# Kernel tuning notes

Hardware: AMD Instinct MI355X
Metric: run time of the kernel (lower is better)

The kernel has to match this reference:

```python
import jax, jax.numpy as jnp
import numpy as np

D_MODEL, HEADS, D_FF = 768, 12, 3072
D_K = D_MODEL // HEADS
EPS = 1e-6


def _norm(x, alpha, bias):
    # NormalizationLayer: scalar alpha/bias, torch.std is unbiased (ddof=1)
    mean = jnp.mean(x, axis=-1, keepdims=True)
    std = jnp.std(x, axis=-1, ddof=1, keepdims=True)
    return alpha * (x - mean) / (std + EPS) + bias


def setup_inputs() -> dict:
    key = jax.random.key(0)
    ks = jax.random.split(key, 16)
    B, S = 2, 4096
    x = jax.random.normal(ks[0], (B, S, D_MODEL), dtype=jnp.float32)
    mask = jax.random.randint(ks[1], (B, 1, 1, S), 0, 2, dtype=jnp.int32)
    w = lambda k, o, i: (jax.random.normal(k, (o, i), dtype=jnp.float32) * 0.02)
    return {
        "x": x, "mask": mask,
        "wq": w(ks[2], D_MODEL, D_MODEL), "bq": jnp.zeros((D_MODEL,), jnp.float32),
        "wk": w(ks[3], D_MODEL, D_MODEL), "bk": jnp.zeros((D_MODEL,), jnp.float32),
        "wv": w(ks[4], D_MODEL, D_MODEL), "bv": jnp.zeros((D_MODEL,), jnp.float32),
        "wo": w(ks[5], D_MODEL, D_MODEL), "bo": jnp.zeros((D_MODEL,), jnp.float32),
        "w1": w(ks[6], D_FF, D_MODEL), "b1": jnp.zeros((D_FF,), jnp.float32),
        "w2": w(ks[7], D_MODEL, D_FF), "b2": jnp.zeros((D_MODEL,), jnp.float32),
        "alpha1": jnp.ones((1,), jnp.float32), "beta1": jnp.ones((1,), jnp.float32),
        "alpha2": jnp.ones((1,), jnp.float32), "beta2": jnp.ones((1,), jnp.float32),
    }


def reference(x, mask, wq, bq, wk, bk, wv, bv, wo, bo, w1, b1, w2, b2,
              alpha1, beta1, alpha2, beta2):
    B, S, _ = x.shape

    # --- residual connection 0: pre-norm + self-attention ---
    h = _norm(x, alpha1, beta1)
    q = (h @ wq.T + bq).reshape(B, S, HEADS, D_K).transpose(0, 2, 1, 3)  # [B,H,S,dk]
    k = (h @ wk.T + bk).reshape(B, S, HEADS, D_K).transpose(0, 2, 1, 3)
    v = (h @ wv.T + bv).reshape(B, S, HEADS, D_K).transpose(0, 2, 1, 3)
    scores = jnp.einsum('bhqd,bhkd->bhqk', q, k) / jnp.sqrt(jnp.float32(D_K))
    scores = jnp.where(mask == 0, jnp.float32(-1e9), scores)
    attn = jax.nn.softmax(scores, axis=-1)
    ctx = jnp.einsum('bhqk,bhkd->bhqd', attn, v)
    ctx = ctx.transpose(0, 2, 1, 3).reshape(B, S, D_MODEL)
    x = x + (ctx @ wo.T + bo)

    # --- residual connection 1: pre-norm + FFN ---
    h = _norm(x, alpha2, beta2)
    ff = jax.nn.relu(h @ w1.T + b1) @ w2.T + b2
    return x + ff
```

## Files before the change

### kernel.cpp

```cpp
#include <hip/hip_runtime.h>
#include <hip/hip_bf16.h>
#include <math.h>


typedef __hip_bfloat16 bf16;
typedef short short8 __attribute__((ext_vector_type(8)));
typedef short short4v __attribute__((ext_vector_type(4)));
typedef float f32x4 __attribute__((ext_vector_type(4)));

#define MFMA(A, B, C) __builtin_amdgcn_mfma_f32_16x16x32_bf16(A, B, C, 0, 0, 0)

#if __has_builtin(__builtin_amdgcn_exp2f)
#define EXP2(x) __builtin_amdgcn_exp2f(x)
#else
#define EXP2(x) exp2f(x)
#endif

__device__ __forceinline__ void gl_lds16(const void* g, void* l) {
  __builtin_amdgcn_global_load_lds(
      (__attribute__((address_space(1))) void*)g,
      (__attribute__((address_space(3))) void*)l, 16, 0, 0);
}

__device__ __forceinline__ short f2b(float f) {
  bf16 h = __float2bfloat16(f);
  return *reinterpret_cast<short*>(&h);
}

__global__ __launch_bounds__(256)
void prep_all(const float* __restrict__ wq, const float* __restrict__ wk,
              const float* __restrict__ wv, const float* __restrict__ wo,
              const float* __restrict__ w1, const float* __restrict__ w2,
              const float* __restrict__ bq, const float* __restrict__ bk,
              const float* __restrict__ bv, const int* __restrict__ mask,
              bf16* __restrict__ wqkvb, bf16* __restrict__ wob,
              bf16* __restrict__ w1b, bf16* __restrict__ w2b,
              float* __restrict__ bqkv,
              int* __restrict__ pos_g, int* __restrict__ nch_g,
              float* __restrict__ biasc,
              bf16* __restrict__ kc, bf16* __restrict__ vtc)
{
  const int t = threadIdx.x;
  if (blockIdx.x < 2) {
    const int b = blockIdx.x;
    const int* mb = mask + b * 4096;
    __shared__ int lsum[256];
    int loc = 0;
    int mv[16];
#pragma unroll
    for (int j = 0; j < 16; j++) { mv[j] = mb[t * 16 + j] ? 1 : 0; loc += mv[j]; }
    lsum[t] = loc;
    __syncthreads();
    for (int off = 1; off < 256; off <<= 1) {
      int v = (t >= off) ? lsum[t - off] : 0;
      __syncthreads();
      lsum[t] += v;
      __syncthreads();
    }
    const int nvalid = lsum[255];
    int base = lsum[t] - loc;
#pragma unroll
    for (int j = 0; j < 16; j++) {
      pos_g[b * 4096 + t * 16 + j] = mv[j] ? base : -1;
      if (mv[j]) base++;
    }
    const int npad = (nvalid + 63) & ~63;
    if (t == 0) nch_g[b] = npad >> 6;
    for (int i = t; i < 4096; i += 256)
      biasc[b * 4096 + i] = (i < nvalid) ? 0.f : -1e9f;
    const int npv = npad - nvalid;
    if (npv > 0) {
      const int krows = 12 * npv;
      const short8 z = {};
      for (int task = t; task < krows * 8; task += 256) {
        const int rr = task >> 3, cc = task & 7;
        const int hh = rr / npv, r = nvalid + rr % npv;
        *(short8*)&kc[(((long)(b * 12 + hh) * 4096) + r) * 64 + cc * 8] = z;
      }
      const int vrows = 12 * 64;
      for (int task = t; task < vrows * npv; task += 256) {
        const int row = task / npv, j = nvalid + task % npv;
        const int hh = row >> 6, d = row & 63;
        vtc[((long)((b * 12 + hh) * 64 + d)) * 4096 + j] = __float2bfloat16(0.f);
      }
    }
    return;
  }
  const int i = (blockIdx.x - 2) * 256 + t;
  const int W = 147456;
  const int F = 589824;
  const float* src; bf16* dst; int off;
  if (i < W)          { src = wq; dst = wqkvb;           off = i; }
  else if (i < 2*W)   { src = wk; dst = wqkvb + 589824;  off = i - W; }
  else if (i < 3*W)   { src = wv; dst = wqkvb + 1179648; off = i - 2*W; }
  else if (i < 4*W)   { src = wo; dst = wob;             off = i - 3*W; }
  else if (i < 4*W+F) { src = w1; dst = w1b;             off = i - 4*W; }
  else                { src = w2; dst = w2b;             off = i - 4*W - F; }
  float4 v = ((const float4*)src)[off];
  short4v o;
  o.x = f2b(v.x); o.y = f2b(v.y); o.z = f2b(v.z); o.w = f2b(v.w);
  ((short4v*)dst)[off] = o;
  if (i < 2304)
    bqkv[i] = (i < 768) ? bq[i] : (i < 1536 ? bk[i - 768] : bv[i - 1536]);
}

template<typename INT>
__global__ __launch_bounds__(256)
void ln_kernel(const INT* __restrict__ x, bf16* __restrict__ out,
               const float* __restrict__ alpha, const float* __restrict__ beta)
{
  const int row = blockIdx.x;
  const long base = (long)row * 768;
  const int t = threadIdx.x;
  float v[3]; float s = 0.f, ss = 0.f;
#pragma unroll
  for (int i = 0; i < 3; i++) {
    v[i] = (float)x[base + t + i * 256];
    s += v[i]; ss += v[i] * v[i];
  }
#pragma unroll
  for (int off = 32; off > 0; off >>= 1) {
    s  += __shfl_down(s, off);
    ss += __shfl_down(ss, off);
  }
  __shared__ float red[8];
  __shared__ float stats[2];
  const int w = t >> 6;
  if ((t & 63) == 0) { red[w] = s; red[4 + w] = ss; }
  __syncthreads();
  if (t == 0) {
    float S  = red[0] + red[1] + red[2] + red[3];
    float SS = red[4] + red[5] + red[6] + red[7];
    float mean = S * (1.f / 768.f);
    float var = fmaxf((SS - 768.f * mean * mean) * (1.f / 767.f), 0.f);
    stats[0] = mean;
    stats[1] = 1.f / (sqrtf(var) + 1e-6f);
  }
  __syncthreads();
  const float mean = stats[0], rinv = stats[1];
  const float a = alpha[0], b = beta[0];
#pragma unroll
  for (int i = 0; i < 3; i++)
    out[base + t + i * 256] = __float2bfloat16(a * (v[i] - mean) * rinv + b);
}

template<int MODE, int TM, typename RT, typename OUTT>
__global__ __launch_bounds__(256)
void gemm_bt(const bf16* __restrict__ A, const bf16* __restrict__ W,
             const float* __restrict__ bias, const RT* __restrict__ R,
             OUTT* __restrict__ Cout, int M, int N, int K)
{
  constexpr int MI = TM / 32;
  __shared__ __align__(16) bf16 sA[TM * 32];
  __shared__ __align__(16) bf16 sB[128 * 32];
  const int t = threadIdx.x;
  const int w = t >> 6, lane = t & 63;
  const int lr = lane & 15, quad = lane >> 4;
  const int tm = blockIdx.x * TM, tn = blockIdx.y * 128;
  const int wm = (w >> 1) * (MI * 16), wn = (w & 1) * 64;

  const int srow = w * 16 + (lane >> 2);
  const int scol = (lane & 3) * 8;
  const bf16* Ap = A + (long)(tm + srow) * K + scol;
  const bf16* Wp = W + (long)(tn + srow) * K + scol;
  bf16* sAp = &sA[srow * 32 + scol];
  bf16* sBp = &sB[srow * 32 + scol];
  const long half = (long)64 * K;

  f32x4 acc[MI][4] = {};

  for (int kb = 0; kb < K; kb += 32) {
    gl_lds16(Ap + kb, sAp);
    if (TM == 128) gl_lds16(Ap + kb + half, sAp + 64 * 32);
    gl_lds16(Wp + kb, sBp);
    gl_lds16(Wp + kb + half, sBp + 64 * 32);
    __syncthreads();
    short8 af[MI], bfr[4];
#pragma unroll
    for (int i = 0; i < MI; i++)
      af[i] = *(const short8*)&sA[(wm + i * 16 + lr) * 32 + quad * 8];
#pragma unroll
    for (int j = 0; j < 4; j++)
      bfr[j] = *(const short8*)&sB[(wn + j * 16 + lr) * 32 + quad * 8];
#pragma unroll
    for (int i = 0; i < MI; i++)
#pragma unroll
      for (int j = 0; j < 4; j++)
        acc[i][j] = MFMA(af[i], bfr[j], acc[i][j]);
    __syncthreads();
  }

#pragma unroll
  for (int i = 0; i < MI; i++) {
#pragma unroll
    for (int j = 0; j < 4; j++) {
      const int col = tn + wn + j * 16 + lr;
      const float bv = bias[col];
#pragma unroll
      for (int r = 0; r < 4; r++) {
        const int m = tm + wm + i * 16 + quad * 4 + r;
        float vv = acc[i][j][r] + bv;
        if (MODE == 1) vv = fmaxf(vv, 0.f);
        if (MODE == 4) vv += (float)R[(long)m * N + col];
        Cout[(long)m * N + col] = (OUTT)vv;
      }
    }
  }
}

__global__ __launch_bounds__(256)
void gemm_qkv(const bf16* __restrict__ A, const bf16* __restrict__ W,
              const float* __restrict__ bias, const int* __restrict__ pos_g,
              bf16* __restrict__ Qo, bf16* __restrict__ Kc, bf16* __restrict__ Vtc)
{
  const int K = 768;
  __shared__ __align__(16) bf16 sA[128 * 32];
  __shared__ __align__(16) bf16 sB[128 * 32];
  const int t = threadIdx.x;
  const int w = t >> 6, lane = t & 63;
  const int lr = lane & 15, quad = lane >> 4;
  const int tm = blockIdx.x * 128, tn = blockIdx.y * 128;
  const int wm = (w >> 1) * 64, wn = (w & 1) * 64;

  const int srow = w * 16 + (lane >> 2);
  const int scol = (lane & 3) * 8;
  const bf16* Ap = A + (long)(tm + srow) * K + scol;
  const bf16* Wp = W + (long)(tn + srow) * K + scol;
  bf16* sAp = &sA[srow * 32 + scol];
  bf16* sBp = &sB[srow * 32 + scol];
  const long half = (long)64 * K;

  f32x4 acc[4][4] = {};

  for (int kb = 0; kb < K; kb += 32) {
    gl_lds16(Ap + kb, sAp);
    gl_lds16(Ap + kb + half, sAp + 64 * 32);
    gl_lds16(Wp + kb, sBp);
    gl_lds16(Wp + kb + half, sBp + 64 * 32);
    __syncthreads();
    short8 af[4], bfr[4];
#pragma unroll
    for (int i = 0; i < 4; i++)
      af[i] = *(const short8*)&sA[(wm + i * 16 + lr) * 32 + quad * 8];
#pragma unroll
    for (int j = 0; j < 4; j++)
      bfr[j] = *(const short8*)&sB[(wn + j * 16 + lr) * 32 + quad * 8];
#pragma unroll
    for (int i = 0; i < 4; i++)
#pragma unroll
      for (int j = 0; j < 4; j++)
        acc[i][j] = MFMA(af[i], bfr[j], acc[i][j]);
    __syncthreads();
  }

  const int region = (tn >= 1536) ? 2 : (tn >= 768 ? 1 : 0);
#pragma unroll
  for (int i = 0; i < 4; i++) {
#pragma unroll
    for (int j = 0; j < 4; j++) {
      const int col = tn + wn + j * 16 + lr;
      const int c768 = col - region * 768;
      const int hh = c768 >> 6, d = c768 & 63;
      const float bv = bias[col];
#pragma unroll
      for (int r = 0; r < 4; r++) {
        const int m = tm + wm + i * 16 + quad * 4 + r;
        const int bb = m >> 12, sdx = m & 4095;
        float vv = acc[i][j][r] + bv;
        if (region == 0) {
          vv *= 0.18033688011112042f;
          Qo[((long)(bb * 12 + hh) * 4096 + sdx) * 64 + d] = __float2bfloat16(vv);
        } else {
          const int p_ = pos_g[bb * 4096 + sdx];
          if (p_ >= 0) {
            if (region == 1)
              Kc[((long)(bb * 12 + hh) * 4096 + p_) * 64 + d] = __float2bfloat16(vv);
            else
              Vtc[((long)(bb * 12 + hh) * 64 + d) * 4096 + p_] = __float2bfloat16(vv);
          }
        }
      }
    }
  }
}

__global__ __launch_bounds__(256)
void attn_kernel(const bf16* __restrict__ Q, const bf16* __restrict__ Kg,
                 const bf16* __restrict__ Vt, const float* __restrict__ biasc,
                 const int* __restrict__ nch_g, bf16* __restrict__ ctx)
{
  __shared__ __align__(16) bf16 sK[2][64 * 64];
  __shared__ __align__(16) bf16 sV[2][64 * 64];
  __shared__ __align__(16) bf16 sP[4][32 * 64];

  const int t = threadIdx.x, w = t >> 6, lane = t & 63;
  const int lr = lane & 15, quad = lane >> 4;
  const int bh = blockIdx.y, b = bh / 12, hh = bh % 12;
  const int qb = blockIdx.x * 128 + w * 32;
  const long bh_s = (long)bh * 4096;
  const float* bg = biasc + b * 4096;
  const int nch = nch_g[b];
  bf16* sPw = sP[w];

  short8 qf[2][2];
#pragma unroll
  for (int qt = 0; qt < 2; qt++) {
    const bf16* qp = Q + (bh_s + qb + qt * 16 + lr) * 64 + quad * 8;
    qf[qt][0] = *(const short8*)qp;
    qf[qt][1] = *(const short8*)(qp + 32);
  }

  const int rA = w * 16 + (lane >> 3), rB = rA + 8;
  const int c8 = lane & 7;
  const int sigA = ((rA & 15) << 2) + (rA >> 4);
  const int sigB = ((rB & 15) << 2) + (rB >> 4);
  const bf16* kA = Kg + (bh_s + sigA) * 64 + ((c8 ^ (rA & 7)) << 3);
  const bf16* kB = Kg + (bh_s + sigB) * 64 + ((c8 ^ (rB & 7)) << 3);
  const bf16* vA = Vt + ((long)bh * 64 + rA) * 4096 + ((c8 ^ (rA & 7)) << 3);
  const bf16* vB = Vt + ((long)bh * 64 + rB) * 4096 + ((c8 ^ (rB & 7)) << 3);
  const int ldsA = (w * 16) * 64 + lane * 8;
  const int ldsB = ldsA + 8 * 64;

  const int cA = (quad * 8) ^ ((lr & 7) << 3);

  float l_part[2][4] = {};
  f32x4 O[2][4] = {};

  auto stage = [&](int kc, int buf) {
    gl_lds16(kA + (long)kc * 64, &sK[buf][ldsA]);
    gl_lds16(kB + (long)kc * 64, &sK[buf][ldsB]);
    gl_lds16(vA + kc, &sV[buf][ldsA]);
    gl_lds16(vB + kc, &sV[buf][ldsB]);
  };

  auto compute = [&](int kc, int buf, bool dobias) {
    const bf16* Kb = sK[buf];
    const bf16* Vb = sV[buf];
    f32x4 s[2][4] = {};
#pragma unroll
    for (int kt = 0; kt < 4; kt++) {
      const int rowb = (kt * 16 + lr) * 64;
      short8 kfa = *(const short8*)&Kb[rowb + cA];
      short8 kfb = *(const short8*)&Kb[rowb + (cA ^ 32)];
      s[0][kt] = MFMA(qf[0][0], kfa, s[0][kt]);
      s[0][kt] = MFMA(qf[0][1], kfb, s[0][kt]);
      s[1][kt] = MFMA(qf[1][0], kfa, s[1][kt]);
      s[1][kt] = MFMA(qf[1][1], kfb, s[1][kt]);
    }
    float bb0 = 0.f, bb1 = 0.f, bb2 = 0.f, bb3 = 0.f;
    if (dobias) {
      const float4 b4 = *(const float4*)&bg[kc + lr * 4];
      bb0 = b4.x; bb1 = b4.y; bb2 = b4.z; bb3 = b4.w;
    }
#pragma unroll
    for (int qt = 0; qt < 2; qt++) {
#pragma unroll
      for (int r = 0; r < 4; r++) {
        float p0, p1, p2, p3;
        if (dobias) {
          p0 = EXP2(s[qt][0][r] + bb0); p1 = EXP2(s[qt][1][r] + bb1);
          p2 = EXP2(s[qt][2][r] + bb2); p3 = EXP2(s[qt][3][r] + bb3);
        } else {
          p0 = EXP2(s[qt][0][r]); p1 = EXP2(s[qt][1][r]);
          p2 = EXP2(s[qt][2][r]); p3 = EXP2(s[qt][3][r]);
        }
        l_part[qt][r] += (p0 + p1) + (p2 + p3);
        const int q = qt * 16 + quad * 4 + r;
        short4v pw;
        pw.x = f2b(p0); pw.y = f2b(p1); pw.z = f2b(p2); pw.w = f2b(p3);
        *(short4v*)&sPw[q * 64 + ((lr * 4) ^ ((q & 7) << 3))] = pw;
      }
    }
    short8 pf[2][2];
#pragma unroll
    for (int qt = 0; qt < 2; qt++) {
      const int rowb = (qt * 16 + lr) * 64;
      pf[qt][0] = *(const short8*)&sPw[rowb + cA];
      pf[qt][1] = *(const short8*)&sPw[rowb + (cA ^ 32)];
    }
#pragma unroll
    for (int j = 0; j < 4; j++) {
      const int rowb = (j * 16 + lr) * 64;
      short8 vfa = *(const short8*)&Vb[rowb + cA];
      short8 vfb = *(const short8*)&Vb[rowb + (cA ^ 32)];
      O[0][j] = MFMA(pf[0][0], vfa, O[0][j]);
      O[0][j] = MFMA(pf[0][1], vfb, O[0][j]);
      O[1][j] = MFMA(pf[1][0], vfa, O[1][j]);
      O[1][j] = MFMA(pf[1][1], vfb, O[1][j]);
    }
  };

  stage(0, 0);
  for (int ci = 0; ci < nch - 1; ci++) {
    __syncthreads();
    stage((ci + 1) * 64, (ci + 1) & 1);
    compute(ci * 64, ci & 1, false);
  }
  __syncthreads();
  if (nch > 0) compute((nch - 1) * 64, (nch - 1) & 1, true);

#pragma unroll
  for (int qt = 0; qt < 2; qt++) {
#pragma unroll
    for (int r = 0; r < 4; r++) {
      float l = l_part[qt][r];
#pragma unroll
      for (int off = 1; off < 16; off <<= 1) l += __shfl_xor(l, off, 16);
      const float il = (l > 0.f) ? 1.f / l : 0.f;
      const int q = qb + qt * 16 + quad * 4 + r;
      bf16* cp = ctx + ((long)(b * 4096 + q)) * 768 + hh * 64 + lr;
#pragma unroll
      for (int j = 0; j < 4; j++)
        cp[j * 16] = __float2bfloat16(O[qt][j][r] * il);
    }
  }
}

extern "C" void kernel_launch(void* const* d_in, const int* in_sizes, int n_in,
                              void* d_out, int out_size, void* d_ws, size_t ws_size,
                              hipStream_t stream)
{
  (void)in_sizes; (void)n_in; (void)out_size; (void)ws_size;
  const float* x    = (const float*)d_in[0];
  const int*   mask = (const int*)  d_in[1];
  const float* wq = (const float*)d_in[2];  const float* bq = (const float*)d_in[3];
  const float* wk = (const float*)d_in[4];  const float* bk = (const float*)d_in[5];
  const float* wv = (const float*)d_in[6];  const float* bv = (const float*)d_in[7];
  const float* wo = (const float*)d_in[8];  const float* bo = (const float*)d_in[9];
  const float* w1 = (const float*)d_in[10]; const float* b1 = (const float*)d_in[11];
  const float* w2 = (const float*)d_in[12]; const float* b2 = (const float*)d_in[13];
  const float* alpha1 = (const float*)d_in[14]; const float* beta1 = (const float*)d_in[15];
  const float* alpha2 = (const float*)d_in[16]; const float* beta2 = (const float*)d_in[17];
  float* out = (float*)d_out;

  const long WSZ = (long)768 * 768 * 2;
  const long W1SZ = (long)3072 * 768 * 2;
  const long SZB = (long)8192 * 768 * 2;
  char* ws = (char*)d_ws;
  bf16* wqkvb = (bf16*)(ws);
  bf16* wob = (bf16*)(ws + 3 * WSZ);
  bf16* w1b = (bf16*)(ws + 4 * WSZ);
  bf16* w2b = (bf16*)(ws + 4 * WSZ + W1SZ);
  char* aux = ws + 4 * WSZ + 2 * W1SZ;
  float* bqkv   = (float*)(aux);
  int*   pos_g  = (int*)(aux + 16384);
  float* biasc  = (float*)(aux + 49152);
  int*   nch_g  = (int*)(aux + 81920);
  const long BASE = 16l << 20;
  bf16* h   = (bf16*)(ws + BASE);
  bf16* qws = (bf16*)(ws + BASE + 1 * SZB);
  bf16* kcw = (bf16*)(ws + BASE + 2 * SZB);
  bf16* vtc = (bf16*)(ws + BASE + 3 * SZB);
  bf16* ctx = (bf16*)(ws + BASE + 4 * SZB);
  bf16* x1  = (bf16*)(ws + BASE + 5 * SZB);
  bf16* ff  = qws;

  dim3 blk(256);

  hipLaunchKernelGGL(prep_all, dim3(6914), blk, 0, stream,
                     wq, wk, wv, wo, w1, w2, bq, bk, bv, mask,
                     wqkvb, wob, w1b, w2b, bqkv, pos_g, nch_g, biasc, kcw, vtc);

  hipLaunchKernelGGL((ln_kernel<float>), dim3(8192), blk, 0, stream, x, h, alpha1, beta1);
  hipLaunchKernelGGL(gemm_qkv, dim3(64, 18), blk, 0, stream, h, wqkvb, bqkv, pos_g, qws, kcw, vtc);
  hipLaunchKernelGGL(attn_kernel, dim3(32, 24), blk, 0, stream, qws, kcw, vtc, biasc, nch_g, ctx);
  hipLaunchKernelGGL((gemm_bt<4, 64, float, bf16>), dim3(128, 6), blk, 0, stream, ctx, wob, bo, x, x1, 8192, 768, 768);
  hipLaunchKernelGGL((ln_kernel<bf16>), dim3(8192), blk, 0, stream, x1, h, alpha2, beta2);
  hipLaunchKernelGGL((gemm_bt<1, 128, float, bf16>), dim3(64, 24), blk, 0, stream, h, w1b, b1, (const float*)nullptr, ff, 8192, 3072, 768);
  hipLaunchKernelGGL((gemm_bt<4, 64, bf16, float>), dim3(128, 6), blk, 0, stream, ff, w2b, b2, x1, out, 8192, 768, 3072);
}
```

Baseline: 407.3 us.

## Keep attention probabilities in registers via transposed MFMA and permlane swaps

The attention kernel now computes S^T and O^T by swapping the MFMA operands, then repacks the bf16 probabilities with v_cvt_pk and v_permlane16/32 swaps. This lets them feed the PV MFMA straight from registers instead of taking a round trip through per-wave LDS. The padding bias on the last chunk is replaced by zero-padded K rows, whose exp2(0)=1 contributions are subtracted from the row sum using a stored padding count. s_setprio hints are added around the MFMA sections. The risks are reliance on gfx950-specific permlane instructions and on an exact correction for the padded keys.

```diff
diff --git a/kernel.cpp b/kernel.cpp
--- a/kernel.cpp
+++ b/kernel.cpp
@@ -15,6 +15,15 @@
 #else
 #define EXP2(x) exp2f(x)
 #endif
+
+#define PSWAP32(a, b) asm("v_permlane32_swap_b32 %0, %1" : "+v"(a), "+v"(b))
+#define PSWAP16(a, b) asm("v_permlane16_swap_b32 %0, %1" : "+v"(a), "+v"(b))
+
+__device__ __forceinline__ unsigned cvt_pk(float lo, float hi) {
+  unsigned r;
+  asm("v_cvt_pk_bf16_f32 %0, %1, %2" : "=v"(r) : "v"(lo), "v"(hi));
+  return r;
+}
 
 __device__ __forceinline__ void gl_lds16(const void* g, void* l) {
   __builtin_amdgcn_global_load_lds(
@@ -37,7 +46,6 @@
               bf16* __restrict__ w1b, bf16* __restrict__ w2b,
               float* __restrict__ bqkv,
               int* __restrict__ pos_g, int* __restrict__ nch_g,
-              float* __restrict__ biasc,
               bf16* __restrict__ kc, bf16* __restrict__ vtc)
 {
   const int t = threadIdx.x;
@@ -65,9 +73,7 @@
       if (mv[j]) base++;
     }
     const int npad = (nvalid + 63) & ~63;
-    if (t == 0) nch_g[b] = npad >> 6;
-    for (int i = t; i < 4096; i += 256)
-      biasc[b * 4096 + i] = (i < nvalid) ? 0.f : -1e9f;
+    if (t == 0) { nch_g[b * 2] = npad >> 6; nch_g[b * 2 + 1] = npad - nvalid; }
     const int npv = npad - nvalid;
     if (npv > 0) {
       const int krows = 12 * npv;
@@ -286,21 +292,19 @@
 
 __global__ __launch_bounds__(256)
 void attn_kernel(const bf16* __restrict__ Q, const bf16* __restrict__ Kg,
-                 const bf16* __restrict__ Vt, const float* __restrict__ biasc,
+                 const bf16* __restrict__ Vt,
                  const int* __restrict__ nch_g, bf16* __restrict__ ctx)
 {
   __shared__ __align__(16) bf16 sK[2][64 * 64];
   __shared__ __align__(16) bf16 sV[2][64 * 64];
-  __shared__ __align__(16) bf16 sP[4][32 * 64];
 
   const int t = threadIdx.x, w = t >> 6, lane = t & 63;
   const int lr = lane & 15, quad = lane >> 4;
   const int bh = blockIdx.y, b = bh / 12, hh = bh % 12;
   const int qb = blockIdx.x * 128 + w * 32;
   const long bh_s = (long)bh * 4096;
-  const float* bg = biasc + b * 4096;
-  const int nch = nch_g[b];
-  bf16* sPw = sP[w];
+  const int nch = nch_g[b * 2];
+  const int npv = nch_g[b * 2 + 1];
 
   short8 qf[2][2];
 #pragma unroll
@@ -312,10 +316,8 @@
 
   const int rA = w * 16 + (lane >> 3), rB = rA + 8;
   const int c8 = lane & 7;
-  const int sigA = ((rA & 15) << 2) + (rA >> 4);
-  const int sigB = ((rB & 15) << 2) + (rB >> 4);
-  const bf16* kA = Kg + (bh_s + sigA) * 64 + ((c8 ^ (rA & 7)) << 3);
-  const bf16* kB = Kg + (bh_s + sigB) * 64 + ((c8 ^ (rB & 7)) << 3);
+  const bf16* kA = Kg + (bh_s + rA) * 64 + ((c8 ^ (rA & 7)) << 3);
+  const bf16* kB = Kg + (bh_s + rB) * 64 + ((c8 ^ (rB & 7)) << 3);
   const bf16* vA = Vt + ((long)bh * 64 + rA) * 4096 + ((c8 ^ (rA & 7)) << 3);
   const bf16* vB = Vt + ((long)bh * 64 + rB) * 4096 + ((c8 ^ (rB & 7)) << 3);
   const int ldsA = (w * 16) * 64 + lane * 8;
@@ -323,8 +325,8 @@
 
   const int cA = (quad * 8) ^ ((lr & 7) << 3);
 
-  float l_part[2][4] = {};
-  f32x4 O[2][4] = {};
+  float l_part[2] = {};
+  f32x4 Ot[4][2] = {};
 
   auto stage = [&](int kc, int buf) {
     gl_lds16(kA + (long)kc * 64, &sK[buf][ldsA]);
@@ -333,85 +335,90 @@
     gl_lds16(vB + kc, &sV[buf][ldsB]);
   };
 
-  auto compute = [&](int kc, int buf, bool dobias) {
+  auto compute = [&](int buf) {
     const bf16* Kb = sK[buf];
     const bf16* Vb = sV[buf];
-    f32x4 s[2][4] = {};
+    f32x4 st[4][2] = {};
+    __builtin_amdgcn_s_setprio(1);
 #pragma unroll
     for (int kt = 0; kt < 4; kt++) {
       const int rowb = (kt * 16 + lr) * 64;
       short8 kfa = *(const short8*)&Kb[rowb + cA];
       short8 kfb = *(const short8*)&Kb[rowb + (cA ^ 32)];
-      s[0][kt] = MFMA(qf[0][0], kfa, s[0][kt]);
-      s[0][kt] = MFMA(qf[0][1], kfb, s[0][kt]);
-      s[1][kt] = MFMA(qf[1][0], kfa, s[1][kt]);
-      s[1][kt] = MFMA(qf[1][1], kfb, s[1][kt]);
-    }
-    float bb0 = 0.f, bb1 = 0.f, bb2 = 0.f, bb3 = 0.f;
-    if (dobias) {
-      const float4 b4 = *(const float4*)&bg[kc + lr * 4];
-      bb0 = b4.x; bb1 = b4.y; bb2 = b4.z; bb3 = b4.w;
-    }
+      st[kt][0] = MFMA(kfa, qf[0][0], st[kt][0]);
+      st[kt][0] = MFMA(kfb, qf[0][1], st[kt][0]);
+      st[kt][1] = MFMA(kfa, qf[1][0], st[kt][1]);
+      st[kt][1] = MFMA(kfb, qf[1][1], st[kt][1]);
+    }
+    __builtin_amdgcn_s_setprio(0);
+
+    short8 pf[2][2];
 #pragma unroll
     for (int qt = 0; qt < 2; qt++) {
-#pragma unroll
-      for (int r = 0; r < 4; r++) {
-        float p0, p1, p2, p3;
-        if (dobias) {
-          p0 = EXP2(s[qt][0][r] + bb0); p1 = EXP2(s[qt][1][r] + bb1);
-          p2 = EXP2(s[qt][2][r] + bb2); p3 = EXP2(s[qt][3][r] + bb3);
-        } else {
-          p0 = EXP2(s[qt][0][r]); p1 = EXP2(s[qt][1][r]);
-          p2 = EXP2(s[qt][2][r]); p3 = EXP2(s[qt][3][r]);
+      float p[4][4];
+      float lp = 0.f;
+#pragma unroll
+      for (int kt = 0; kt < 4; kt++) {
+#pragma unroll
+        for (int r = 0; r < 4; r++) {
+          p[kt][r] = EXP2(st[kt][qt][r]);
+          lp += p[kt][r];
         }
-        l_part[qt][r] += (p0 + p1) + (p2 + p3);
-        const int q = qt * 16 + quad * 4 + r;
-        short4v pw;
-        pw.x = f2b(p0); pw.y = f2b(p1); pw.z = f2b(p2); pw.w = f2b(p3);
-        *(short4v*)&sPw[q * 64 + ((lr * 4) ^ ((q & 7) << 3))] = pw;
       }
-    }
-    short8 pf[2][2];
-#pragma unroll
-    for (int qt = 0; qt < 2; qt++) {
-      const int rowb = (qt * 16 + lr) * 64;
-      pf[qt][0] = *(const short8*)&sPw[rowb + cA];
-      pf[qt][1] = *(const short8*)&sPw[rowb + (cA ^ 32)];
-    }
-#pragma unroll
-    for (int j = 0; j < 4; j++) {
-      const int rowb = (j * 16 + lr) * 64;
+      l_part[qt] += lp;
+      unsigned u00 = cvt_pk(p[0][0], p[0][1]), u01 = cvt_pk(p[0][2], p[0][3]);
+      unsigned u10 = cvt_pk(p[1][0], p[1][1]), u11 = cvt_pk(p[1][2], p[1][3]);
+      unsigned u20 = cvt_pk(p[2][0], p[2][1]), u21 = cvt_pk(p[2][2], p[2][3]);
+      unsigned u30 = cvt_pk(p[3][0], p[3][1]), u31 = cvt_pk(p[3][2], p[3][3]);
+      PSWAP32(u00, u10); PSWAP32(u01, u11);
+      PSWAP32(u20, u30); PSWAP32(u21, u31);
+      PSWAP16(u00, u10); PSWAP16(u01, u11);
+      PSWAP16(u20, u30); PSWAP16(u21, u31);
+      union { unsigned u[4]; short8 s8; } fa, fb;
+      fa.u[0] = u00; fa.u[1] = u01; fa.u[2] = u10; fa.u[3] = u11;
+      fb.u[0] = u20; fb.u[1] = u21; fb.u[2] = u30; fb.u[3] = u31;
+      pf[qt][0] = fa.s8;
+      pf[qt][1] = fb.s8;
+    }
+
+    __builtin_amdgcn_s_setprio(1);
+#pragma unroll
+    for (int dt = 0; dt < 4; dt++) {
+      const int rowb = (dt * 16 + lr) * 64;
       short8 vfa = *(const short8*)&Vb[rowb + cA];
       short8 vfb = *(const short8*)&Vb[rowb + (cA ^ 32)];
-      O[0][j] = MFMA(pf[0][0], vfa, O[0][j]);
-      O[0][j] = MFMA(pf[0][1], vfb, O[0][j]);
-      O[1][j] = MFMA(pf[1][0], vfa, O[1][j]);
-      O[1][j] = MFMA(pf[1][1], vfb, O[1][j]);
-    }
+      Ot[dt][0] = MFMA(vfa, pf[0][0], Ot[dt][0]);
+      Ot[dt][0] = MFMA(vfb, pf[0][1], Ot[dt][0]);
+      Ot[dt][1] = MFMA(vfa, pf[1][0], Ot[dt][1]);
+      Ot[dt][1] = MFMA(vfb, pf[1][1], Ot[dt][1]);
+    }
+    __builtin_amdgcn_s_setprio(0);
   };
 
   stage(0, 0);
-  for (int ci = 0; ci < nch - 1; ci++) {
-    __syncthreads();
-    stage((ci + 1) * 64, (ci + 1) & 1);
-    compute(ci * 64, ci & 1, false);
-  }
-  __syncthreads();
-  if (nch > 0) compute((nch - 1) * 64, (nch - 1) & 1, true);
+  for (int ci = 0; ci < nch; ci++) {
+    __syncthreads();
+    if (ci + 1 < nch) stage((ci + 1) * 64, (ci + 1) & 1);
+    compute(ci & 1);
+  }
 
 #pragma unroll
   for (int qt = 0; qt < 2; qt++) {
-#pragma unroll
-    for (int r = 0; r < 4; r++) {
-      float l = l_part[qt][r];
-#pragma unroll
-      for (int off = 1; off < 16; off <<= 1) l += __shfl_xor(l, off, 16);
-      const float il = (l > 0.f) ? 1.f / l : 0.f;
-      const int q = qb + qt * 16 + quad * 4 + r;
-      bf16* cp = ctx + ((long)(b * 4096 + q)) * 768 + hh * 64 + lr;
-#pragma unroll
-      for (int j = 0; j < 4; j++)
-        cp[j * 16] = __float2bfloat16(O[qt][j][r] * il);
+    float l = l_part[qt];
+    l += __shfl_xor(l, 16);
+    l += __shfl_xor(l, 32);
+    l -= (float)npv;
+    const float il = (l > 0.f) ? 1.f / l : 0.f;
+    const int q = qb + qt * 16 + lr;
+    bf16* cp = ctx + ((long)(b * 4096 + q)) * 768 + hh * 64 + quad * 4;
+#pragma unroll
+    for (int dt = 0; dt < 4; dt++) {
+      short4v ov;
+      ov.x = f2b(Ot[dt][qt][0] * il);
+      ov.y = f2b(Ot[dt][qt][1] * il);
+      ov.z = f2b(Ot[dt][qt][2] * il);
+      ov.w = f2b(Ot[dt][qt][3] * il);
+      *(short4v*)(cp + dt * 16) = ov;
     }
   }
 }
@@ -444,7 +451,6 @@
   char* aux = ws + 4 * WSZ + 2 * W1SZ;
   float* bqkv   = (float*)(aux);
   int*   pos_g  = (int*)(aux + 16384);
-  float* biasc  = (float*)(aux + 49152);
   int*   nch_g  = (int*)(aux + 81920);
   const long BASE = 16l << 20;
   bf16* h   = (bf16*)(ws + BASE);
@@ -459,11 +465,11 @@
 
   hipLaunchKernelGGL(prep_all, dim3(6914), blk, 0, stream,
                      wq, wk, wv, wo, w1, w2, bq, bk, bv, mask,
-                     wqkvb, wob, w1b, w2b, bqkv, pos_g, nch_g, biasc, kcw, vtc);
+                     wqkvb, wob, w1b, w2b, bqkv, pos_g, nch_g, kcw, vtc);
 
   hipLaunchKernelGGL((ln_kernel<float>), dim3(8192), blk, 0, stream, x, h, alpha1, beta1);
   hipLaunchKernelGGL(gemm_qkv, dim3(64, 18), blk, 0, stream, h, wqkvb, bqkv, pos_g, qws, kcw, vtc);
-  hipLaunchKernelGGL(attn_kernel, dim3(32, 24), blk, 0, stream, qws, kcw, vtc, biasc, nch_g, ctx);
+  hipLaunchKernelGGL(attn_kernel, dim3(32, 24), blk, 0, stream, qws, kcw, vtc, nch_g, ctx);
   hipLaunchKernelGGL((gemm_bt<4, 64, float, bf16>), dim3(128, 6), blk, 0, stream, ctx, wob, bo, x, x1, 8192, 768, 768);
   hipLaunchKernelGGL((ln_kernel<bf16>), dim3(8192), blk, 0, stream, x1, h, alpha2, beta2);
   hipLaunchKernelGGL((gemm_bt<1, 128, float, bf16>), dim3(64, 24), blk, 0, stream, h, w1b, b1, (const float*)nullptr, ff, 8192, 3072, 768);
```

Measured after the change: 405.8 us. No clear change (-0.4%).
